# Kernel tuning notes

Hardware: AMD Instinct MI355X
Metric: run time of the kernel (lower is better)

## Reference

```python
import jax, jax.numpy as jnp
import numpy as np

B, D, FV, EMB, HID, E = 256, 1000, 300, 128, 128, 32000
NUM_LAYERS = 3


def _gcn_layer(h, src, tgt, W, b):
    # PyG GCNConv (add_self_loops=True, normalize=True) over N = h.shape[0] nodes.
    # NOTE: edges only reference nodes [0, D) (faithful to original forward),
    # but self-loops exist for all N nodes.
    N = h.shape[0]
    h = h @ W.T  # [N, out]
    deg = jnp.ones((N,), h.dtype).at[tgt].add(1.0)  # self-loop + in-degree
    dinv = deg ** -0.5
    coef = dinv[src] * dinv[tgt]  # [E]
    agg = jnp.zeros_like(h).at[tgt].add(h[src] * coef[:, None])
    agg = agg + h * (dinv * dinv)[:, None]  # self-loop messages
    return agg + b


def setup_inputs() -> dict:
    key = jax.random.key(0)
    ks = jax.random.split(key, 10)
    inp = {
        "X_num": jax.random.normal(ks[0], (B, 800), jnp.float32),
        "X_cat": jax.random.normal(ks[1], (B, 200), jnp.float32),
        "V": jax.random.normal(ks[2], (D, FV), jnp.float32),
        "edge_index": jax.random.randint(ks[3], (2, E), 0, D, jnp.int32),
        "W_embed": jax.random.normal(ks[4], (EMB, FV), jnp.float32) / np.sqrt(FV),
        "b_embed": jnp.zeros((EMB,), jnp.float32),
        "W0": jax.random.normal(ks[5], (HID, EMB), jnp.float32) / np.sqrt(EMB),
        "b0": jnp.zeros((HID,), jnp.float32),
        "W1": jax.random.normal(ks[6], (HID, HID), jnp.float32) / np.sqrt(HID),
        "b1": jnp.zeros((HID,), jnp.float32),
        "W2": jax.random.normal(ks[7], (HID, HID), jnp.float32) / np.sqrt(HID),
        "b2": jnp.zeros((HID,), jnp.float32),
    }
    return inp


def reference(X_num, X_cat, V, edge_index, W_embed, b_embed, W0, b0, W1, b1, W2, b2):
    x = jnp.concatenate([X_num, X_cat], axis=1)  # [B, D]
    emb = V @ W_embed.T + b_embed  # [D, EMB]
    h = x[:, :, None] * emb[None, :, :]  # [B, D, EMB]
    h = h.reshape(B * D, EMB)
    src, tgt = edge_index[0], edge_index[1]
    for W, b in ((W0, b0), (W1, b1), (W2, b2)):
        h = jax.nn.relu(_gcn_layer(h, src, tgt, W, b))
    h = h.reshape(B, D, HID)
    return h.mean(axis=1)  # conv_pool_method == 'mean'
```

## Files before the change

### kernel.cpp

```cpp
#include <hip/hip_runtime.h>
#include <hip/hip_bf16.h>

#define B_N 256
#define D_N 1000
#define H_N 128
#define E_N 32000
#define CAP 128

typedef unsigned int uint32;
typedef unsigned short u16;
typedef __attribute__((ext_vector_type(8))) short bf16x8;
typedef __attribute__((ext_vector_type(4))) float f32x4;

__device__ __forceinline__ u16 f2bf(float f) {
    union { float f; uint32 u; } v; v.f = f;
    return (u16)((v.u + 0x7fffu + ((v.u >> 16) & 1u)) >> 16);
}
__device__ __forceinline__ uint32 pk2(float lo, float hi) {
    __hip_bfloat162 h = __float22bfloat162_rn(make_float2(lo, hi));
    union { __hip_bfloat162 h; uint32 u; } v; v.h = h; return v.u;
}
__device__ __forceinline__ float asf(uint32 u) {
    union { uint32 u; float f; } v; v.u = u; return v.f;
}
__device__ __forceinline__ float rl(float x) { return x > 0.f ? x : 0.f; }

__device__ __forceinline__ void ld8g(const float* __restrict__ p, int kbase, float v[8]) {
    if (kbase + 8 <= 300) {
        float4 a = *(const float4*)p, b = *(const float4*)(p + 4);
        v[0] = a.x; v[1] = a.y; v[2] = a.z; v[3] = a.w;
        v[4] = b.x; v[5] = b.y; v[6] = b.z; v[7] = b.w;
    } else {
#pragma unroll
        for (int j = 0; j < 8; ++j) v[j] = (kbase + j < 300) ? p[j] : 0.f;
    }
}

__device__ __forceinline__ bf16x8 mk_h1(float xv, uint4 e, float4 bl, float4 bh) {
    float v0 = rl(fmaf(xv, asf(e.x << 16), bl.x));
    float v1 = rl(fmaf(xv, asf(e.x & 0xffff0000u), bl.y));
    float v2 = rl(fmaf(xv, asf(e.y << 16), bl.z));
    float v3 = rl(fmaf(xv, asf(e.y & 0xffff0000u), bl.w));
    float v4 = rl(fmaf(xv, asf(e.z << 16), bh.x));
    float v5 = rl(fmaf(xv, asf(e.z & 0xffff0000u), bh.y));
    float v6 = rl(fmaf(xv, asf(e.w << 16), bh.z));
    float v7 = rl(fmaf(xv, asf(e.w & 0xffff0000u), bh.w));
    uint4 pk = { pk2(v0, v1), pk2(v2, v3), pk2(v4, v5), pk2(v6, v7) };
    return *(const bf16x8*)&pk;
}

__global__ void k_prep(const float* __restrict__ V, const float* __restrict__ W_embed,
                       const float* __restrict__ b_embed, const float* __restrict__ W0,
                       const float* __restrict__ Xn, const float* __restrict__ Xc,
                       const float* __restrict__ W1, const float* __restrict__ W2,
                       int* __restrict__ deg,
                       u16* __restrict__ w1h, u16* __restrict__ w2h,
                       u16* __restrict__ E1h, float* __restrict__ t0,
                       float* __restrict__ out) {
    __shared__ __align__(16) u16 sW0[128 * 128];
    __shared__ __align__(16) u16 sWc[128 * 64];
    __shared__ __align__(16) u16 sVc[16 * 64];
    __shared__ __align__(16) u16 sT[16 * 128];

    int bid = blockIdx.x, tid = threadIdx.x;
    if (bid >= 63) {
        if (bid < 127) {
            int i = (bid - 63) * 256 + tid;
            w1h[i] = f2bf(W1[i]); w2h[i] = f2bf(W2[i]);
        } else if (bid < 255) {
            int i = (bid - 127) * 256 + tid;
            out[i] = 0.f;
        } else {
            for (int j = tid; j < D_N; j += 256) deg[j] = 0;
        }
        return;
    }

    const int wave = tid >> 6, lane = tid & 63;
    const int quad = lane >> 4, l15 = lane & 15;
    const int nh = wave;
    const int dbase = bid * 16;

#pragma unroll
    for (int ii = 0; ii < 8; ++ii) {
        int idx = tid + ii * 256;
        int row = idx >> 4, g = idx & 15;
        float4 a = *(const float4*)(W0 + row * 128 + g * 8);
        float4 b = *(const float4*)(W0 + row * 128 + g * 8 + 4);
        uint4 pk = { pk2(a.x, a.y), pk2(a.z, a.w), pk2(b.x, b.y), pk2(b.z, b.w) };
        *(uint4*)&sW0[row * 128 + ((g ^ (row & 7)) << 3)] = pk;
    }

    f32x4 accA[2];
#pragma unroll
    for (int n = 0; n < 2; ++n) { accA[n][0] = 0.f; accA[n][1] = 0.f; accA[n][2] = 0.f; accA[n][3] = 0.f; }

    for (int ck = 0; ck < 5; ++ck) {
        int k0 = ck * 64;
        if (tid < 128) {
            int row = tid >> 3, seg = tid & 7;
            int d = dbase + row; int dc = d < D_N ? d : D_N - 1;
            int kk = k0 + seg * 8;
            float v[8]; ld8g(V + dc * 300 + kk, kk, v);
            uint4 pk = { pk2(v[0], v[1]), pk2(v[2], v[3]), pk2(v[4], v[5]), pk2(v[6], v[7]) };
            *(uint4*)&sVc[row * 64 + ((seg ^ (row & 7)) << 3)] = pk;
        }
#pragma unroll
        for (int gg = 0; gg < 4; ++gg) {
            int idx = tid + gg * 256;
            int row = idx >> 3, g = idx & 7;
            int kk = k0 + g * 8;
            float v[8]; ld8g(W_embed + row * 300 + kk, kk, v);
            uint4 pk = { pk2(v[0], v[1]), pk2(v[2], v[3]), pk2(v[4], v[5]), pk2(v[6], v[7]) };
            *(uint4*)&sWc[row * 64 + ((g ^ (row & 7)) << 3)] = pk;
        }
        __syncthreads();
#pragma unroll
        for (int ksb = 0; ksb < 2; ++ksb) {
            int g = ksb * 4 + quad;
            bf16x8 av = *(const bf16x8*)&sVc[l15 * 64 + ((g ^ (l15 & 7)) << 3)];
#pragma unroll
            for (int n = 0; n < 2; ++n) {
                int br = nh * 32 + n * 16 + l15;
                bf16x8 bv = *(const bf16x8*)&sWc[br * 64 + ((g ^ (br & 7)) << 3)];
                accA[n] = __builtin_amdgcn_mfma_f32_16x16x32_bf16(av, bv, accA[n], 0, 0, 0);
            }
        }
        __syncthreads();
    }

    {
        const int odd = l15 & 1;
#pragma unroll
        for (int n = 0; n < 2; ++n) {
            float bb = b_embed[nh * 32 + n * 16 + l15];
            float v0 = accA[n][0] + bb, v1 = accA[n][1] + bb;
            float v2 = accA[n][2] + bb, v3 = accA[n][3] + bb;
            float t0_ = __shfl_xor(v0, 1), t1_ = __shfl_xor(v1, 1);
            float t2_ = __shfl_xor(v2, 1), t3_ = __shfl_xor(v3, 1);
            float lo0 = odd ? t2_ : v0, hi0 = odd ? v2 : t0_;
            float lo1 = odd ? t3_ : v1, hi1 = odd ? v3 : t1_;
            int r0 = quad * 4 + (odd ? 2 : 0);
            int r1 = r0 + 1;
            int ce = nh * 32 + n * 16 + (l15 & ~1);
            *(uint32*)&sT[r0 * 128 + (((ce >> 3) ^ (r0 & 7)) << 3) + (ce & 7)] = pk2(lo0, hi0);
            *(uint32*)&sT[r1 * 128 + (((ce >> 3) ^ (r1 & 7)) << 3) + (ce & 7)] = pk2(lo1, hi1);
        }
    }
    __syncthreads();

    f32x4 accB[2];
#pragma unroll
    for (int n = 0; n < 2; ++n) { accB[n][0] = 0.f; accB[n][1] = 0.f; accB[n][2] = 0.f; accB[n][3] = 0.f; }
#pragma unroll
    for (int ks = 0; ks < 4; ++ks) {
        int g = ks * 4 + quad;
        bf16x8 av = *(const bf16x8*)&sT[l15 * 128 + ((g ^ (l15 & 7)) << 3)];
#pragma unroll
        for (int n = 0; n < 2; ++n) {
            int br = nh * 32 + n * 16 + l15;
            bf16x8 bv = *(const bf16x8*)&sW0[br * 128 + ((g ^ (br & 7)) << 3)];
            accB[n] = __builtin_amdgcn_mfma_f32_16x16x32_bf16(av, bv, accB[n], 0, 0, 0);
        }
    }

#pragma unroll
    for (int i = 0; i < 4; ++i) {
        int r = quad * 4 + i;
        int d = dbase + r;
        if (d < D_N) {
            float x0 = (d < 800) ? Xn[d] : Xc[d - 800];
#pragma unroll
            for (int n = 0; n < 2; ++n) {
                int col = nh * 32 + n * 16 + l15;
                float e1 = accB[n][i];
                E1h[d * H_N + col] = f2bf(e1);
                t0[d * H_N + col] = x0 * e1;
            }
        }
    }
}

__global__ void k_layer(const float* __restrict__ t_in, const float* __restrict__ bias,
                        const float* __restrict__ Wn, const int* __restrict__ deg,
                        const int* __restrict__ es,
                        float* __restrict__ t_out, float* out, int pool) {
    __shared__ float sh[128];
    int d = blockIdx.x, e = threadIdx.x;
    float di = rsqrtf(1.f + (float)deg[d]);
    float acc = t_in[d * H_N + e] * di * di;
    int n = deg[d]; if (n > CAP) n = CAP;
    const int* row = es + d * CAP;
    int i = 0;
    for (; i + 4 <= n; i += 4) {
        int a0 = row[i], a1 = row[i + 1], a2 = row[i + 2], a3 = row[i + 3];
        float c0 = rsqrtf(1.f + (float)deg[a0]);
        float c1 = rsqrtf(1.f + (float)deg[a1]);
        float c2 = rsqrtf(1.f + (float)deg[a2]);
        float c3 = rsqrtf(1.f + (float)deg[a3]);
        acc += di * (c0 * t_in[a0 * H_N + e] + c1 * t_in[a1 * H_N + e] +
                     c2 * t_in[a2 * H_N + e] + c3 * t_in[a3 * H_N + e]);
    }
    for (; i < n; ++i) {
        int s = row[i];
        acc += di * rsqrtf(1.f + (float)deg[s]) * t_in[s * H_N + e];
    }
    float h = rl(acc + bias[e]);
    if (pool) { atomicAdd(&out[e], h * (1.0f / 1000.0f)); return; }
    sh[e] = h;
    __syncthreads();
    const float4* hr = (const float4*)sh;
    const float4* wr = (const float4*)(Wn + e * 128);
    float s = 0.f;
#pragma unroll 8
    for (int k = 0; k < 32; ++k) {
        float4 a = hr[k], w = wr[k];
        s += a.x * w.x + a.y * w.y + a.z * w.z + a.w * w.w;
    }
    t_out[d * H_N + e] = s;
}

__global__ __launch_bounds__(256, 2)
void k_big(const float* __restrict__ Xn, const float* __restrict__ Xc,
           const u16* __restrict__ E1h, const u16* __restrict__ w1h,
           const u16* __restrict__ w2h, const float* __restrict__ b0,
           const float* __restrict__ b1, const float* __restrict__ b2,
           const int* __restrict__ eidx, int* __restrict__ deg,
           int* __restrict__ es, float* __restrict__ out) {
    __shared__ __align__(16) u16 sA[128 * 128];
    __shared__ __align__(16) u16 sB[128 * 128];

    if (blockIdx.x < 125) {
        int e = blockIdx.x * 256 + threadIdx.x;
        int s = eidx[e], t = eidx[E_N + e];
        int pos = atomicAdd(&deg[t], 1);
        if (pos < CAP) es[t * CAP + pos] = s;
        return;
    }
    const int cb = blockIdx.x - 125;
    const int tid = threadIdx.x;
    const int wave = tid >> 6, lane = tid & 63;
    const int quad = lane >> 4, l15 = lane & 15;
    const int pr = cb >> 3;
    const int bi0 = 1 + 2 * pr;
    const int bi1 = 2 + 2 * pr;
    const int wr1 = bi1 < B_N;
    const int bi1c = wr1 ? bi1 : B_N - 1;
    const int mbase = ((cb & 7) << 7) + wave * 32;
    u16* hw = sA + wave * (32 * 128);

    {
        const uint4* w1v = (const uint4*)w1h;
        const uint4* w2v = (const uint4*)w2h;
#pragma unroll
        for (int i = 0; i < 8; ++i) {
            int idx = tid + i * 256;
            int row = idx >> 4, g = idx & 15;
            int off = row * 128 + ((g ^ (row & 7)) << 3);
            *(uint4*)&sA[off] = w1v[idx];
            *(uint4*)&sB[off] = w2v[idx];
        }
    }

    const int rA = mbase + l15;  const int rAc = rA < D_N ? rA : D_N - 1;
    const int rB = rA + 16;      const int rBc = rB < D_N ? rB : D_N - 1;
    const float xv0A = (rAc < 800) ? Xn[bi0 * 800 + rAc] : Xc[bi0 * 200 + rAc - 800];
    const float xv0B = (rBc < 800) ? Xn[bi0 * 800 + rBc] : Xc[bi0 * 200 + rBc - 800];
    const float xv1A = (rAc < 800) ? Xn[bi1c * 800 + rAc] : Xc[bi1c * 200 + rAc - 800];
    const float xv1B = (rBc < 800) ? Xn[bi1c * 800 + rBc] : Xc[bi1c * 200 + rBc - 800];

    f32x4 acc0[2][8], acc1[2][8];
#pragma unroll
    for (int rt = 0; rt < 2; ++rt)
#pragma unroll
        for (int n = 0; n < 8; ++n) {
            acc0[rt][n][0] = 0.f; acc0[rt][n][1] = 0.f; acc0[rt][n][2] = 0.f; acc0[rt][n][3] = 0.f;
            acc1[rt][n][0] = 0.f; acc1[rt][n][1] = 0.f; acc1[rt][n][2] = 0.f; acc1[rt][n][3] = 0.f;
        }

    __syncthreads();

#pragma unroll
    for (int ks = 0; ks < 4; ++ks) {
        const int k8 = ks * 4 + quad;
        uint4 eA = *(const uint4*)(E1h + rAc * H_N + k8 * 8);
        uint4 eB = *(const uint4*)(E1h + rBc * H_N + k8 * 8);
        float4 bl = *(const float4*)(b0 + k8 * 8);
        float4 bh = *(const float4*)(b0 + k8 * 8 + 4);
        bf16x8 a0A = mk_h1(xv0A, eA, bl, bh);
        bf16x8 a0B = mk_h1(xv0B, eB, bl, bh);
        bf16x8 a1A = mk_h1(xv1A, eA, bl, bh);
        bf16x8 a1B = mk_h1(xv1B, eB, bl, bh);
#pragma unroll
        for (int n = 0; n < 8; ++n) {
            int br = n * 16 + l15;
            bf16x8 bw = *(const bf16x8*)&sA[br * 128 + ((k8 ^ (br & 7)) << 3)];
            acc0[0][n] = __builtin_amdgcn_mfma_f32_16x16x32_bf16(a0A, bw, acc0[0][n], 0, 0, 0);
            acc0[1][n] = __builtin_amdgcn_mfma_f32_16x16x32_bf16(a0B, bw, acc0[1][n], 0, 0, 0);
            acc1[0][n] = __builtin_amdgcn_mfma_f32_16x16x32_bf16(a1A, bw, acc1[0][n], 0, 0, 0);
            acc1[1][n] = __builtin_amdgcn_mfma_f32_16x16x32_bf16(a1B, bw, acc1[1][n], 0, 0, 0);
        }
    }

    __syncthreads();

    const int rem = D_N - mbase;
    const int odd = l15 & 1;

#pragma unroll
    for (int bsel = 0; bsel < 2; ++bsel) {
        f32x4 (*accp)[8] = bsel ? acc1 : acc0;
        int bi = bsel ? bi1 : bi0;
        int wr = bsel ? wr1 : 1;

#pragma unroll
        for (int rt = 0; rt < 2; ++rt)
#pragma unroll
            for (int n = 0; n < 8; ++n) {
                float bg = b1[n * 16 + l15];
                float v0 = rl(accp[rt][n][0] + bg);
                float v1 = rl(accp[rt][n][1] + bg);
                float v2 = rl(accp[rt][n][2] + bg);
                float v3 = rl(accp[rt][n][3] + bg);
                float t0_ = __shfl_xor(v0, 1), t1_ = __shfl_xor(v1, 1);
                float t2_ = __shfl_xor(v2, 1), t3_ = __shfl_xor(v3, 1);
                float lo0 = odd ? t2_ : v0, hi0 = odd ? v2 : t0_;
                float lo1 = odd ? t3_ : v1, hi1 = odd ? v3 : t1_;
                int r0 = rt * 16 + quad * 4 + (odd ? 2 : 0);
                int r1 = r0 + 1;
                int ce = n * 16 + (l15 & ~1);
                *(uint32*)&hw[r0 * 128 + (((ce >> 3) ^ (r0 & 7)) << 3) + (ce & 7)] = pk2(lo0, hi0);
                *(uint32*)&hw[r1 * 128 + (((ce >> 3) ^ (r1 & 7)) << 3) + (ce & 7)] = pk2(lo1, hi1);
            }

#pragma unroll
        for (int rt = 0; rt < 2; ++rt)
#pragma unroll
            for (int n = 0; n < 8; ++n) {
                accp[rt][n][0] = 0.f; accp[rt][n][1] = 0.f;
                accp[rt][n][2] = 0.f; accp[rt][n][3] = 0.f;
            }
#pragma unroll
        for (int ks = 0; ks < 4; ++ks) {
            int k8 = ks * 4 + quad;
            int m0 = l15, m1 = 16 + l15;
            bf16x8 a0 = *(const bf16x8*)&hw[m0 * 128 + ((k8 ^ (m0 & 7)) << 3)];
            bf16x8 a1 = *(const bf16x8*)&hw[m1 * 128 + ((k8 ^ (m1 & 7)) << 3)];
#pragma unroll
            for (int n = 0; n < 8; ++n) {
                int br = n * 16 + l15;
                bf16x8 bw = *(const bf16x8*)&sB[br * 128 + ((k8 ^ (br & 7)) << 3)];
                accp[0][n] = __builtin_amdgcn_mfma_f32_16x16x32_bf16(a0, bw, accp[0][n], 0, 0, 0);
                accp[1][n] = __builtin_amdgcn_mfma_f32_16x16x32_bf16(a1, bw, accp[1][n], 0, 0, 0);
            }
        }

#pragma unroll
        for (int n = 0; n < 8; ++n) {
            float bg = b2[n * 16 + l15];
            float cs = 0.f;
#pragma unroll
            for (int rt = 0; rt < 2; ++rt)
#pragma unroll
                for (int i = 0; i < 4; ++i) {
                    int r32 = rt * 16 + quad * 4 + i;
                    float v = rl(accp[rt][n][i] + bg);
                    if (r32 < rem) cs += v;
                }
            cs += __shfl_xor(cs, 16);
            cs += __shfl_xor(cs, 32);
            if (lane < 16 && wr)
                atomicAdd(&out[bi * H_N + n * 16 + l15], cs * (1.0f / 1000.0f));
        }
    }
}

extern "C" void kernel_launch(void* const* d_in, const int* in_sizes, int n_in,
                              void* d_out, int out_size, void* d_ws, size_t ws_size,
                              hipStream_t stream) {
    const float* Xn = (const float*)d_in[0];
    const float* Xc = (const float*)d_in[1];
    const float* V = (const float*)d_in[2];
    const int* eidx = (const int*)d_in[3];
    const float* W_embed = (const float*)d_in[4];
    const float* b_embed = (const float*)d_in[5];
    const float* W0 = (const float*)d_in[6];
    const float* b0 = (const float*)d_in[7];
    const float* W1 = (const float*)d_in[8];
    const float* b1 = (const float*)d_in[9];
    const float* W2 = (const float*)d_in[10];
    const float* b2 = (const float*)d_in[11];
    float* out = (float*)d_out;

    char* p = (char*)d_ws;
    auto alloc = [&](size_t bytes) -> char* {
        char* r = p;
        p += (bytes + 255) & ~(size_t)255;
        return r;
    };
    u16*   E1h = (u16*)  alloc(D_N * H_N * 2);
    float* t0  = (float*)alloc(D_N * H_N * 4);
    float* t1  = (float*)alloc(D_N * H_N * 4);
    float* t2  = (float*)alloc(D_N * H_N * 4);
    u16*   w1h = (u16*)  alloc(H_N * H_N * 2);
    u16*   w2h = (u16*)  alloc(H_N * H_N * 2);
    int*   deg = (int*)  alloc(D_N * 4);
    int*   es  = (int*)  alloc(D_N * CAP * 4);

    k_prep<<<dim3(256), dim3(256), 0, stream>>>(V, W_embed, b_embed, W0, Xn, Xc,
                                                W1, W2, deg, w1h, w2h, E1h, t0, out);
    k_big<<<dim3(1149), dim3(256), 0, stream>>>(Xn, Xc, E1h, w1h, w2h, b0, b1, b2,
                                                eidx, deg, es, out);
    k_layer<<<dim3(1000), dim3(128), 0, stream>>>(t0, b0, W1, deg, es, t1, out, 0);
    k_layer<<<dim3(1000), dim3(128), 0, stream>>>(t1, b1, W2, deg, es, t2, out, 0);
    k_layer<<<dim3(1000), dim3(128), 0, stream>>>(t2, b2, (const float*)nullptr, deg, es,
                                                  (float*)nullptr, out, 1);
}
```

Baseline: 186.6 us.

## Process four batch items per block and fold edge bucketing into compute blocks

The large fused kernel now handles four batch items per block, in two passes of two, instead of two. The edge-bucketing work is no longer done by separate blocks and is folded into the first 125 compute blocks. The grid shrinks from 1149 to 512 blocks. This amortizes the shared-memory loads of the W1/W2 weights and the per-block setup over more batch items, and removes the early-return edge-only blocks. The cost is extra barriers and a reload of sA (overwritten by the hidden tile) in the second pass, fewer blocks to spread across CUs, and a longer serial path in the blocks that also do edge work.

```diff
diff --git a/kernel.cpp b/kernel.cpp
--- a/kernel.cpp
+++ b/kernel.cpp
@@ -230,24 +230,36 @@
     __shared__ __align__(16) u16 sA[128 * 128];
     __shared__ __align__(16) u16 sB[128 * 128];
 
-    if (blockIdx.x < 125) {
-        int e = blockIdx.x * 256 + threadIdx.x;
+    const int cb = blockIdx.x;
+    const int tid = threadIdx.x;
+    const int wave = tid >> 6, lane = tid & 63;
+    const int quad = lane >> 4, l15 = lane & 15;
+
+    if (cb < 125) {
+        int e = cb * 256 + tid;
         int s = eidx[e], t = eidx[E_N + e];
         int pos = atomicAdd(&deg[t], 1);
         if (pos < CAP) es[t * CAP + pos] = s;
-        return;
-    }
-    const int cb = blockIdx.x - 125;
-    const int tid = threadIdx.x;
-    const int wave = tid >> 6, lane = tid & 63;
-    const int quad = lane >> 4, l15 = lane & 15;
-    const int pr = cb >> 3;
-    const int bi0 = 1 + 2 * pr;
-    const int bi1 = 2 + 2 * pr;
-    const int wr1 = bi1 < B_N;
-    const int bi1c = wr1 ? bi1 : B_N - 1;
-    const int mbase = ((cb & 7) << 7) + wave * 32;
+    }
+
+    const int g = cb >> 3;
+    const int chunk = cb & 7;
+    const int bibase = 1 + 4 * g;
+    const int mbase = (chunk << 7) + wave * 32;
     u16* hw = sA + wave * (32 * 128);
+
+    const int rA = mbase + l15;  const int rAc = rA < D_N ? rA : D_N - 1;
+    const int rB = rA + 16;      const int rBc = rB < D_N ? rB : D_N - 1;
+
+    float xv[4][2]; int bok[4];
+#pragma unroll
+    for (int q = 0; q < 4; ++q) {
+        int bi = bibase + q;
+        bok[q] = bi < B_N;
+        int bic = bok[q] ? bi : B_N - 1;
+        xv[q][0] = (rAc < 800) ? Xn[bic * 800 + rAc] : Xc[bic * 200 + rAc - 800];
+        xv[q][1] = (rBc < 800) ? Xn[bic * 800 + rBc] : Xc[bic * 200 + rBc - 800];
+    }
 
     {
         const uint4* w1v = (const uint4*)w1h;
@@ -255,122 +267,129 @@
 #pragma unroll
         for (int i = 0; i < 8; ++i) {
             int idx = tid + i * 256;
-            int row = idx >> 4, g = idx & 15;
-            int off = row * 128 + ((g ^ (row & 7)) << 3);
+            int row = idx >> 4, gg = idx & 15;
+            int off = row * 128 + ((gg ^ (row & 7)) << 3);
             *(uint4*)&sA[off] = w1v[idx];
             *(uint4*)&sB[off] = w2v[idx];
         }
     }
-
-    const int rA = mbase + l15;  const int rAc = rA < D_N ? rA : D_N - 1;
-    const int rB = rA + 16;      const int rBc = rB < D_N ? rB : D_N - 1;
-    const float xv0A = (rAc < 800) ? Xn[bi0 * 800 + rAc] : Xc[bi0 * 200 + rAc - 800];
-    const float xv0B = (rBc < 800) ? Xn[bi0 * 800 + rBc] : Xc[bi0 * 200 + rBc - 800];
-    const float xv1A = (rAc < 800) ? Xn[bi1c * 800 + rAc] : Xc[bi1c * 200 + rAc - 800];
-    const float xv1B = (rBc < 800) ? Xn[bi1c * 800 + rBc] : Xc[bi1c * 200 + rBc - 800];
-
-    f32x4 acc0[2][8], acc1[2][8];
-#pragma unroll
-    for (int rt = 0; rt < 2; ++rt)
-#pragma unroll
-        for (int n = 0; n < 8; ++n) {
-            acc0[rt][n][0] = 0.f; acc0[rt][n][1] = 0.f; acc0[rt][n][2] = 0.f; acc0[rt][n][3] = 0.f;
-            acc1[rt][n][0] = 0.f; acc1[rt][n][1] = 0.f; acc1[rt][n][2] = 0.f; acc1[rt][n][3] = 0.f;
-        }
-
-    __syncthreads();
-
-#pragma unroll
-    for (int ks = 0; ks < 4; ++ks) {
-        const int k8 = ks * 4 + quad;
-        uint4 eA = *(const uint4*)(E1h + rAc * H_N + k8 * 8);
-        uint4 eB = *(const uint4*)(E1h + rBc * H_N + k8 * 8);
-        float4 bl = *(const float4*)(b0 + k8 * 8);
-        float4 bh = *(const float4*)(b0 + k8 * 8 + 4);
-        bf16x8 a0A = mk_h1(xv0A, eA, bl, bh);
-        bf16x8 a0B = mk_h1(xv0B, eB, bl, bh);
-        bf16x8 a1A = mk_h1(xv1A, eA, bl, bh);
-        bf16x8 a1B = mk_h1(xv1B, eB, bl, bh);
-#pragma unroll
-        for (int n = 0; n < 8; ++n) {
-            int br = n * 16 + l15;
-            bf16x8 bw = *(const bf16x8*)&sA[br * 128 + ((k8 ^ (br & 7)) << 3)];
-            acc0[0][n] = __builtin_amdgcn_mfma_f32_16x16x32_bf16(a0A, bw, acc0[0][n], 0, 0, 0);
-            acc0[1][n] = __builtin_amdgcn_mfma_f32_16x16x32_bf16(a0B, bw, acc0[1][n], 0, 0, 0);
-            acc1[0][n] = __builtin_amdgcn_mfma_f32_16x16x32_bf16(a1A, bw, acc1[0][n], 0, 0, 0);
-            acc1[1][n] = __builtin_amdgcn_mfma_f32_16x16x32_bf16(a1B, bw, acc1[1][n], 0, 0, 0);
-        }
-    }
-
     __syncthreads();
 
     const int rem = D_N - mbase;
     const int odd = l15 & 1;
 
-#pragma unroll
-    for (int bsel = 0; bsel < 2; ++bsel) {
-        f32x4 (*accp)[8] = bsel ? acc1 : acc0;
-        int bi = bsel ? bi1 : bi0;
-        int wr = bsel ? wr1 : 1;
-
+    for (int p = 0; p < 2; ++p) {
+        if (p == 1) {
+            __syncthreads();
+            const uint4* w1v = (const uint4*)w1h;
+#pragma unroll
+            for (int i = 0; i < 8; ++i) {
+                int idx = tid + i * 256;
+                int row = idx >> 4, gg = idx & 15;
+                *(uint4*)&sA[row * 128 + ((gg ^ (row & 7)) << 3)] = w1v[idx];
+            }
+            __syncthreads();
+        }
+        const int q0 = 2 * p, q1 = 2 * p + 1;
+
+        f32x4 acc0[2][8], acc1[2][8];
 #pragma unroll
         for (int rt = 0; rt < 2; ++rt)
 #pragma unroll
             for (int n = 0; n < 8; ++n) {
-                float bg = b1[n * 16 + l15];
-                float v0 = rl(accp[rt][n][0] + bg);
-                float v1 = rl(accp[rt][n][1] + bg);
-                float v2 = rl(accp[rt][n][2] + bg);
-                float v3 = rl(accp[rt][n][3] + bg);
-                float t0_ = __shfl_xor(v0, 1), t1_ = __shfl_xor(v1, 1);
-                float t2_ = __shfl_xor(v2, 1), t3_ = __shfl_xor(v3, 1);
-                float lo0 = odd ? t2_ : v0, hi0 = odd ? v2 : t0_;
-                float lo1 = odd ? t3_ : v1, hi1 = odd ? v3 : t1_;
-                int r0 = rt * 16 + quad * 4 + (odd ? 2 : 0);
-                int r1 = r0 + 1;
-                int ce = n * 16 + (l15 & ~1);
-                *(uint32*)&hw[r0 * 128 + (((ce >> 3) ^ (r0 & 7)) << 3) + (ce & 7)] = pk2(lo0, hi0);
-                *(uint32*)&hw[r1 * 128 + (((ce >> 3) ^ (r1 & 7)) << 3) + (ce & 7)] = pk2(lo1, hi1);
-            }
-
-#pragma unroll
-        for (int rt = 0; rt < 2; ++rt)
-#pragma unroll
-            for (int n = 0; n < 8; ++n) {
-                accp[rt][n][0] = 0.f; accp[rt][n][1] = 0.f;
-                accp[rt][n][2] = 0.f; accp[rt][n][3] = 0.f;
-            }
+                acc0[rt][n][0] = 0.f; acc0[rt][n][1] = 0.f; acc0[rt][n][2] = 0.f; acc0[rt][n][3] = 0.f;
+                acc1[rt][n][0] = 0.f; acc1[rt][n][1] = 0.f; acc1[rt][n][2] = 0.f; acc1[rt][n][3] = 0.f;
+            }
+
 #pragma unroll
         for (int ks = 0; ks < 4; ++ks) {
-            int k8 = ks * 4 + quad;
-            int m0 = l15, m1 = 16 + l15;
-            bf16x8 a0 = *(const bf16x8*)&hw[m0 * 128 + ((k8 ^ (m0 & 7)) << 3)];
-            bf16x8 a1 = *(const bf16x8*)&hw[m1 * 128 + ((k8 ^ (m1 & 7)) << 3)];
+            const int k8 = ks * 4 + quad;
+            uint4 eA = *(const uint4*)(E1h + rAc * H_N + k8 * 8);
+            uint4 eB = *(const uint4*)(E1h + rBc * H_N + k8 * 8);
+            float4 bl = *(const float4*)(b0 + k8 * 8);
+            float4 bh = *(const float4*)(b0 + k8 * 8 + 4);
+            bf16x8 a0A = mk_h1(xv[q0][0], eA, bl, bh);
+            bf16x8 a0B = mk_h1(xv[q0][1], eB, bl, bh);
+            bf16x8 a1A = mk_h1(xv[q1][0], eA, bl, bh);
+            bf16x8 a1B = mk_h1(xv[q1][1], eB, bl, bh);
 #pragma unroll
             for (int n = 0; n < 8; ++n) {
                 int br = n * 16 + l15;
-                bf16x8 bw = *(const bf16x8*)&sB[br * 128 + ((k8 ^ (br & 7)) << 3)];
-                accp[0][n] = __builtin_amdgcn_mfma_f32_16x16x32_bf16(a0, bw, accp[0][n], 0, 0, 0);
-                accp[1][n] = __builtin_amdgcn_mfma_f32_16x16x32_bf16(a1, bw, accp[1][n], 0, 0, 0);
-            }
-        }
-
-#pragma unroll
-        for (int n = 0; n < 8; ++n) {
-            float bg = b2[n * 16 + l15];
-            float cs = 0.f;
+                bf16x8 bw = *(const bf16x8*)&sA[br * 128 + ((k8 ^ (br & 7)) << 3)];
+                acc0[0][n] = __builtin_amdgcn_mfma_f32_16x16x32_bf16(a0A, bw, acc0[0][n], 0, 0, 0);
+                acc0[1][n] = __builtin_amdgcn_mfma_f32_16x16x32_bf16(a0B, bw, acc0[1][n], 0, 0, 0);
+                acc1[0][n] = __builtin_amdgcn_mfma_f32_16x16x32_bf16(a1A, bw, acc1[0][n], 0, 0, 0);
+                acc1[1][n] = __builtin_amdgcn_mfma_f32_16x16x32_bf16(a1B, bw, acc1[1][n], 0, 0, 0);
+            }
+        }
+
+        __syncthreads();
+
+#pragma unroll
+        for (int bsel = 0; bsel < 2; ++bsel) {
+            f32x4 (*accp)[8] = bsel ? acc1 : acc0;
+            int q = bsel ? q1 : q0;
+            int bi = bibase + q;
+
 #pragma unroll
             for (int rt = 0; rt < 2; ++rt)
 #pragma unroll
-                for (int i = 0; i < 4; ++i) {
-                    int r32 = rt * 16 + quad * 4 + i;
-                    float v = rl(accp[rt][n][i] + bg);
-                    if (r32 < rem) cs += v;
+                for (int n = 0; n < 8; ++n) {
+                    float bg = b1[n * 16 + l15];
+                    float v0 = rl(accp[rt][n][0] + bg);
+                    float v1 = rl(accp[rt][n][1] + bg);
+                    float v2 = rl(accp[rt][n][2] + bg);
+                    float v3 = rl(accp[rt][n][3] + bg);
+                    float t0_ = __shfl_xor(v0, 1), t1_ = __shfl_xor(v1, 1);
+                    float t2_ = __shfl_xor(v2, 1), t3_ = __shfl_xor(v3, 1);
+                    float lo0 = odd ? t2_ : v0, hi0 = odd ? v2 : t0_;
+                    float lo1 = odd ? t3_ : v1, hi1 = odd ? v3 : t1_;
+                    int r0 = rt * 16 + quad * 4 + (odd ? 2 : 0);
+                    int r1 = r0 + 1;
+                    int ce = n * 16 + (l15 & ~1);
+                    *(uint32*)&hw[r0 * 128 + (((ce >> 3) ^ (r0 & 7)) << 3) + (ce & 7)] = pk2(lo0, hi0);
+                    *(uint32*)&hw[r1 * 128 + (((ce >> 3) ^ (r1 & 7)) << 3) + (ce & 7)] = pk2(lo1, hi1);
                 }
-            cs += __shfl_xor(cs, 16);
-            cs += __shfl_xor(cs, 32);
-            if (lane < 16 && wr)
-                atomicAdd(&out[bi * H_N + n * 16 + l15], cs * (1.0f / 1000.0f));
+
+#pragma unroll
+            for (int rt = 0; rt < 2; ++rt)
+#pragma unroll
+                for (int n = 0; n < 8; ++n) {
+                    accp[rt][n][0] = 0.f; accp[rt][n][1] = 0.f;
+                    accp[rt][n][2] = 0.f; accp[rt][n][3] = 0.f;
+                }
+#pragma unroll
+            for (int ks = 0; ks < 4; ++ks) {
+                int k8 = ks * 4 + quad;
+                int m0 = l15, m1 = 16 + l15;
+                bf16x8 a0 = *(const bf16x8*)&hw[m0 * 128 + ((k8 ^ (m0 & 7)) << 3)];
+                bf16x8 a1 = *(const bf16x8*)&hw[m1 * 128 + ((k8 ^ (m1 & 7)) << 3)];
+#pragma unroll
+                for (int n = 0; n < 8; ++n) {
+                    int br = n * 16 + l15;
+                    bf16x8 bw = *(const bf16x8*)&sB[br * 128 + ((k8 ^ (br & 7)) << 3)];
+                    accp[0][n] = __builtin_amdgcn_mfma_f32_16x16x32_bf16(a0, bw, accp[0][n], 0, 0, 0);
+                    accp[1][n] = __builtin_amdgcn_mfma_f32_16x16x32_bf16(a1, bw, accp[1][n], 0, 0, 0);
+                }
+            }
+
+#pragma unroll
+            for (int n = 0; n < 8; ++n) {
+                float bg = b2[n * 16 + l15];
+                float cs = 0.f;
+#pragma unroll
+                for (int rt = 0; rt < 2; ++rt)
+#pragma unroll
+                    for (int i = 0; i < 4; ++i) {
+                        int r32 = rt * 16 + quad * 4 + i;
+                        float v = rl(accp[rt][n][i] + bg);
+                        if (r32 < rem) cs += v;
+                    }
+                cs += __shfl_xor(cs, 16);
+                cs += __shfl_xor(cs, 32);
+                if (lane < 16 && bok[q])
+                    atomicAdd(&out[bi * H_N + n * 16 + l15], cs * (1.0f / 1000.0f));
+            }
         }
     }
 }
@@ -409,8 +428,8 @@
 
     k_prep<<<dim3(256), dim3(256), 0, stream>>>(V, W_embed, b_embed, W0, Xn, Xc,
                                                 W1, W2, deg, w1h, w2h, E1h, t0, out);
-    k_big<<<dim3(1149), dim3(256), 0, stream>>>(Xn, Xc, E1h, w1h, w2h, b0, b1, b2,
-                                                eidx, deg, es, out);
+    k_big<<<dim3(512), dim3(256), 0, stream>>>(Xn, Xc, E1h, w1h, w2h, b0, b1, b2,
+                                               eidx, deg, es, out);
     k_layer<<<dim3(1000), dim3(128), 0, stream>>>(t0, b0, W1, deg, es, t1, out, 0);
     k_layer<<<dim3(1000), dim3(128), 0, stream>>>(t1, b1, W2, deg, es, t2, out, 0);
     k_layer<<<dim3(1000), dim3(128), 0, stream>>>(t2, b2, (const float*)nullptr, deg, es,
```

Result: slower. 224.9 us (+20.5%).

## Fuse edge bucketing and three node-layer kernels into one persistent grid-barrier kernel

Applied to the files above, without the earlier changes.

Moves edge bucketing out of k_big and merges it with the three row-0 GCN layer kernels into a single 125-block persistent kernel. A software global barrier built on agent-scope atomics and a magic-value handshake separates the phases. This removes two kernel launches and their gaps, and the pool layer now accumulates per block before a single atomic. The cost is that the row-0 chain uses only 125 blocks and relies on all of them being co-resident for the spin barrier; it still runs serially after k_big on the same stream.

```diff
diff --git a/kernel.cpp b/kernel.cpp
--- a/kernel.cpp
+++ b/kernel.cpp
@@ -6,6 +6,8 @@
 #define H_N 128
 #define E_N 32000
 #define CAP 128
+#define CBLK 125
+#define MAGIC 0x5eed5eed
 
 typedef unsigned int uint32;
 typedef unsigned short u16;
@@ -53,7 +55,7 @@
                        const float* __restrict__ b_embed, const float* __restrict__ W0,
                        const float* __restrict__ Xn, const float* __restrict__ Xc,
                        const float* __restrict__ W1, const float* __restrict__ W2,
-                       int* __restrict__ deg,
+                       int* __restrict__ deg, int* __restrict__ bar,
                        u16* __restrict__ w1h, u16* __restrict__ w2h,
                        u16* __restrict__ E1h, float* __restrict__ t0,
                        float* __restrict__ out) {
@@ -72,6 +74,7 @@
             out[i] = 0.f;
         } else {
             for (int j = tid; j < D_N; j += 256) deg[j] = 0;
+            if (tid < 16) bar[tid] = 0;
         }
         return;
     }
@@ -181,63 +184,16 @@
     }
 }
 
-__global__ void k_layer(const float* __restrict__ t_in, const float* __restrict__ bias,
-                        const float* __restrict__ Wn, const int* __restrict__ deg,
-                        const int* __restrict__ es,
-                        float* __restrict__ t_out, float* out, int pool) {
-    __shared__ float sh[128];
-    int d = blockIdx.x, e = threadIdx.x;
-    float di = rsqrtf(1.f + (float)deg[d]);
-    float acc = t_in[d * H_N + e] * di * di;
-    int n = deg[d]; if (n > CAP) n = CAP;
-    const int* row = es + d * CAP;
-    int i = 0;
-    for (; i + 4 <= n; i += 4) {
-        int a0 = row[i], a1 = row[i + 1], a2 = row[i + 2], a3 = row[i + 3];
-        float c0 = rsqrtf(1.f + (float)deg[a0]);
-        float c1 = rsqrtf(1.f + (float)deg[a1]);
-        float c2 = rsqrtf(1.f + (float)deg[a2]);
-        float c3 = rsqrtf(1.f + (float)deg[a3]);
-        acc += di * (c0 * t_in[a0 * H_N + e] + c1 * t_in[a1 * H_N + e] +
-                     c2 * t_in[a2 * H_N + e] + c3 * t_in[a3 * H_N + e]);
-    }
-    for (; i < n; ++i) {
-        int s = row[i];
-        acc += di * rsqrtf(1.f + (float)deg[s]) * t_in[s * H_N + e];
-    }
-    float h = rl(acc + bias[e]);
-    if (pool) { atomicAdd(&out[e], h * (1.0f / 1000.0f)); return; }
-    sh[e] = h;
-    __syncthreads();
-    const float4* hr = (const float4*)sh;
-    const float4* wr = (const float4*)(Wn + e * 128);
-    float s = 0.f;
-#pragma unroll 8
-    for (int k = 0; k < 32; ++k) {
-        float4 a = hr[k], w = wr[k];
-        s += a.x * w.x + a.y * w.y + a.z * w.z + a.w * w.w;
-    }
-    t_out[d * H_N + e] = s;
-}
-
 __global__ __launch_bounds__(256, 2)
 void k_big(const float* __restrict__ Xn, const float* __restrict__ Xc,
            const u16* __restrict__ E1h, const u16* __restrict__ w1h,
            const u16* __restrict__ w2h, const float* __restrict__ b0,
            const float* __restrict__ b1, const float* __restrict__ b2,
-           const int* __restrict__ eidx, int* __restrict__ deg,
-           int* __restrict__ es, float* __restrict__ out) {
+           float* __restrict__ out) {
     __shared__ __align__(16) u16 sA[128 * 128];
     __shared__ __align__(16) u16 sB[128 * 128];
 
-    if (blockIdx.x < 125) {
-        int e = blockIdx.x * 256 + threadIdx.x;
-        int s = eidx[e], t = eidx[E_N + e];
-        int pos = atomicAdd(&deg[t], 1);
-        if (pos < CAP) es[t * CAP + pos] = s;
-        return;
-    }
-    const int cb = blockIdx.x - 125;
+    const int cb = blockIdx.x;
     const int tid = threadIdx.x;
     const int wave = tid >> 6, lane = tid & 63;
     const int quad = lane >> 4, l15 = lane & 15;
@@ -373,6 +329,104 @@
                 atomicAdd(&out[bi * H_N + n * 16 + l15], cs * (1.0f / 1000.0f));
         }
     }
+}
+
+__global__ __launch_bounds__(256, 2)
+void k_chain(const int* __restrict__ eidx, int* __restrict__ deg,
+             int* __restrict__ es, const float* __restrict__ t0,
+             float* __restrict__ t1, float* __restrict__ t2,
+             const float* __restrict__ b0, const float* __restrict__ b1,
+             const float* __restrict__ b2, const float* __restrict__ W1,
+             const float* __restrict__ W2, int* bar, float* __restrict__ out) {
+    __shared__ float shf[256];
+    const int tid = threadIdx.x, bid = blockIdx.x;
+    const int half = tid >> 7, e = tid & 127;
+
+    if (bid == 0 && tid == 0)
+        __hip_atomic_store(bar, MAGIC, __ATOMIC_RELEASE, __HIP_MEMORY_SCOPE_AGENT);
+
+    {
+        int i = bid * 256 + tid;
+        int s = eidx[i], t = eidx[E_N + i];
+        int pos = atomicAdd(&deg[t], 1);
+        if (pos < CAP) es[t * CAP + pos] = s;
+    }
+
+#define GBAR(c)                                                                      \
+    __syncthreads();                                                                 \
+    if (tid == 0) {                                                                  \
+        while (__hip_atomic_load(bar, __ATOMIC_ACQUIRE, __HIP_MEMORY_SCOPE_AGENT)    \
+               != MAGIC) __builtin_amdgcn_s_sleep(2);                                \
+        __threadfence();                                                             \
+        __hip_atomic_fetch_add(bar + (c), 1, __ATOMIC_ACQ_REL,                       \
+                               __HIP_MEMORY_SCOPE_AGENT);                            \
+        while (__hip_atomic_load(bar + (c), __ATOMIC_ACQUIRE,                        \
+                                 __HIP_MEMORY_SCOPE_AGENT) < CBLK)                   \
+            __builtin_amdgcn_s_sleep(2);                                             \
+    }                                                                                \
+    __syncthreads();
+
+    GBAR(1)
+
+    for (int layer = 0; layer < 2; ++layer) {
+        const float* tin  = layer ? t1 : t0;
+        float*       tout = layer ? t2 : t1;
+        const float* bb   = layer ? b1 : b0;
+        const float* Wn   = layer ? W2 : W1;
+        for (int it = 0; it < 4; ++it) {
+            int d = (bid * 4 + it) * 2 + half;
+            float di = rsqrtf(1.f + (float)deg[d]);
+            float acc = tin[d * H_N + e] * di * di;
+            int n = deg[d]; if (n > CAP) n = CAP;
+            const int* row = es + d * CAP;
+            int i = 0;
+            for (; i + 4 <= n; i += 4) {
+                int a0 = row[i], a1 = row[i + 1], a2 = row[i + 2], a3 = row[i + 3];
+                float c0 = rsqrtf(1.f + (float)deg[a0]);
+                float c1 = rsqrtf(1.f + (float)deg[a1]);
+                float c2 = rsqrtf(1.f + (float)deg[a2]);
+                float c3 = rsqrtf(1.f + (float)deg[a3]);
+                acc += di * (c0 * tin[a0 * H_N + e] + c1 * tin[a1 * H_N + e] +
+                             c2 * tin[a2 * H_N + e] + c3 * tin[a3 * H_N + e]);
+            }
+            for (; i < n; ++i) {
+                int s = row[i];
+                acc += di * rsqrtf(1.f + (float)deg[s]) * tin[s * H_N + e];
+            }
+            float h = rl(acc + bb[e]);
+            shf[tid] = h;
+            __syncthreads();
+            const float4* hr = (const float4*)(shf + half * 128);
+            const float4* wr = (const float4*)(Wn + e * 128);
+            float s = 0.f;
+#pragma unroll 8
+            for (int k = 0; k < 32; ++k) {
+                float4 a = hr[k], w = wr[k];
+                s += a.x * w.x + a.y * w.y + a.z * w.z + a.w * w.w;
+            }
+            tout[d * H_N + e] = s;
+            __syncthreads();
+        }
+        if (layer == 0) { GBAR(2) } else { GBAR(3) }
+    }
+
+    {
+        float accp = 0.f;
+        for (int it = 0; it < 4; ++it) {
+            int d = (bid * 4 + it) * 2 + half;
+            float di = rsqrtf(1.f + (float)deg[d]);
+            float acc = t2[d * H_N + e] * di * di;
+            int n = deg[d]; if (n > CAP) n = CAP;
+            const int* row = es + d * CAP;
+            for (int i = 0; i < n; ++i) {
+                int s = row[i];
+                acc += di * rsqrtf(1.f + (float)deg[s]) * t2[s * H_N + e];
+            }
+            accp += rl(acc + b2[e]);
+        }
+        atomicAdd(&out[e], accp * (1.0f / 1000.0f));
+    }
+#undef GBAR
 }
 
 extern "C" void kernel_launch(void* const* d_in, const int* in_sizes, int n_in,
@@ -406,13 +460,11 @@
     u16*   w2h = (u16*)  alloc(H_N * H_N * 2);
     int*   deg = (int*)  alloc(D_N * 4);
     int*   es  = (int*)  alloc(D_N * CAP * 4);
+    int*   bar = (int*)  alloc(64);
 
     k_prep<<<dim3(256), dim3(256), 0, stream>>>(V, W_embed, b_embed, W0, Xn, Xc,
-                                                W1, W2, deg, w1h, w2h, E1h, t0, out);
-    k_big<<<dim3(1149), dim3(256), 0, stream>>>(Xn, Xc, E1h, w1h, w2h, b0, b1, b2,
-                                                eidx, deg, es, out);
-    k_layer<<<dim3(1000), dim3(128), 0, stream>>>(t0, b0, W1, deg, es, t1, out, 0);
-    k_layer<<<dim3(1000), dim3(128), 0, stream>>>(t1, b1, W2, deg, es, t2, out, 0);
-    k_layer<<<dim3(1000), dim3(128), 0, stream>>>(t2, b2, (const float*)nullptr, deg, es,
-                                                  (float*)nullptr, out, 1);
-}
+                                                W1, W2, deg, bar, w1h, w2h, E1h, t0, out);
+    k_big<<<dim3(1024), dim3(256), 0, stream>>>(Xn, Xc, E1h, w1h, w2h, b0, b1, b2, out);
+    k_chain<<<dim3(CBLK), dim3(256), 0, stream>>>(eidx, deg, es, t0, t1, t2,
+                                                  b0, b1, b2, W1, W2, bar, out);
+}
```

Result: slower. 268.6 us (+44.0%).
